# Performance work log

Measured on AMD Instinct MI355X. Metric: run time of the kernel, lower is better.

Reference implementation:

```python
import jax, jax.numpy as jnp
import numpy as np

B, S, SM, D, H, DFF = 4, 1024, 1024, 1024, 16, 4096
HD = D // H
EPS = 1e-5


def _ln(x, g, b):
    mu = jnp.mean(x, axis=-1, keepdims=True)
    var = jnp.var(x, axis=-1, keepdims=True)
    return (x - mu) * jax.lax.rsqrt(var + EPS) * g + b


def setup_inputs() -> dict:
    key = jax.random.key(0)
    ks = jax.random.split(key, 20)
    w = lambda k, shp: (0.02 * jax.random.normal(k, shp, dtype=jnp.float32))
    return {
        "tgt": jax.random.normal(ks[0], (B, S, D), dtype=jnp.float32),
        "memory": jax.random.normal(ks[1], (B, SM, D), dtype=jnp.float32),
        # self-attn (no bias)
        "Wq": w(ks[2], (D, D)), "Wk": w(ks[3], (D, D)),
        "Wv": w(ks[4], (D, D)), "Wo": w(ks[5], (D, D)),
        # cross-attn nn.MultiheadAttention params
        "mha_in_w": w(ks[6], (3 * D, D)), "mha_in_b": jnp.zeros((3 * D,), jnp.float32),
        "mha_out_w": w(ks[7], (D, D)), "mha_out_b": jnp.zeros((D,), jnp.float32),
        # FFN
        "W1": w(ks[8], (DFF, D)), "b1": jnp.zeros((DFF,), jnp.float32),
        "W2": w(ks[9], (D, DFF)), "b2": jnp.zeros((D,), jnp.float32),
        # LayerNorms
        "g1": jnp.ones((D,), jnp.float32), "be1": jnp.zeros((D,), jnp.float32),
        "g2": jnp.ones((D,), jnp.float32), "be2": jnp.zeros((D,), jnp.float32),
        "g3": jnp.ones((D,), jnp.float32), "be3": jnp.zeros((D,), jnp.float32),
    }


def _self_attn(x, Wq, Wk, Wv, Wo):
    b, s, d = x.shape
    q = (x @ Wq.T).reshape(b, s, H, HD).transpose(0, 2, 1, 3)  # [B,H,S,hd]
    k = (x @ Wk.T).reshape(b, s, H, HD).transpose(0, 2, 1, 3)
    v = (x @ Wv.T).reshape(b, s, H, HD).transpose(0, 2, 1, 3)
    scores = jnp.einsum('bhqd,bhkd->bhqk', q, k) / jnp.sqrt(jnp.float32(HD))
    mask = jnp.triu(jnp.ones((s, s), dtype=bool), k=1)  # diagonal = full_S - S + 1 = 1
    scores = jnp.where(mask, -jnp.inf, scores)
    attn = jax.nn.softmax(scores, axis=-1)
    out = jnp.einsum('bhqk,bhkd->bhqd', attn, v).transpose(0, 2, 1, 3).reshape(b, s, d)
    return out @ Wo.T, k, v


def _cross_attn(q_in, kv_in, in_w, in_b, out_w, out_b):
    Wq, Wk, Wv = jnp.split(in_w, 3, axis=0)
    bq, bk, bv = jnp.split(in_b, 3, axis=0)
    b, s, d = q_in.shape
    sm = kv_in.shape[1]
    q = (q_in @ Wq.T + bq).reshape(b, s, H, HD).transpose(0, 2, 1, 3)
    k = (kv_in @ Wk.T + bk).reshape(b, sm, H, HD).transpose(0, 2, 1, 3)
    v = (kv_in @ Wv.T + bv).reshape(b, sm, H, HD).transpose(0, 2, 1, 3)
    scores = jnp.einsum('bhqd,bhkd->bhqk', q, k) / jnp.sqrt(jnp.float32(HD))
    attn = jax.nn.softmax(scores, axis=-1)
    out = jnp.einsum('bhqk,bhkd->bhqd', attn, v).transpose(0, 2, 1, 3).reshape(b, s, d)
    return out @ out_w.T + out_b


def reference(tgt, memory, Wq, Wk, Wv, Wo, mha_in_w, mha_in_b, mha_out_w, mha_out_b,
              W1, b1, W2, b2, g1, be1, g2, be2, g3, be3):
    # dropout = 0 (eval mode)
    sa_out, sa_k, sa_v = _self_attn(_ln(tgt, g1, be1), Wq, Wk, Wv, Wo)
    x = tgt + sa_out
    ca_out = _cross_attn(_ln(x, g2, be2), memory, mha_in_w, mha_in_b, mha_out_w, mha_out_b)
    x = x + ca_out
    ff = jax.nn.relu(_ln(x, g3, be3) @ W1.T + b1) @ W2.T + b2
    x = x + ff
    return x, sa_k, sa_v
```

## Files before the change

kernel.cpp:

```cpp
#include <hip/hip_runtime.h>

typedef __bf16 bf16_t;
typedef unsigned int u32;
typedef __attribute__((ext_vector_type(8))) __bf16 bf16x8;
typedef __attribute__((ext_vector_type(4))) __bf16 bf16x4;
typedef __attribute__((ext_vector_type(4))) float f32x4;


__device__ __forceinline__ bf16x8 load8f(const float* f) {
    float4 a = *(const float4*)f;
    float4 b = *(const float4*)(f + 4);
    bf16x8 r;
    r[0] = (bf16_t)a.x; r[1] = (bf16_t)a.y; r[2] = (bf16_t)a.z; r[3] = (bf16_t)a.w;
    r[4] = (bf16_t)b.x; r[5] = (bf16_t)b.y; r[6] = (bf16_t)b.z; r[7] = (bf16_t)b.w;
    return r;
}

__device__ __forceinline__ void gll16(const void* g, const void* l) {
    __builtin_amdgcn_global_load_lds(
        (const __attribute__((address_space(1))) u32*)(unsigned long long)g,
        (__attribute__((address_space(3))) u32*)(unsigned int)(unsigned long long)l,
        16, 0, 0);
}

__global__ __launch_bounds__(256) void conv_kernel(
    const float* __restrict__ Wq, const float* __restrict__ Wk,
    const float* __restrict__ Wv, const float* __restrict__ Wo,
    const float* __restrict__ Wio, const float* __restrict__ Woo,
    const float* __restrict__ W1, const float* __restrict__ W2,
    const float* __restrict__ mem, bf16_t* __restrict__ dst)
{
    long e = ((long)blockIdx.x * 256 + threadIdx.x) * 8;
    const float* s; long o;
    if      (e <  1048576) { s = Wq;  o = e; }
    else if (e <  2097152) { s = Wk;  o = e -  1048576; }
    else if (e <  3145728) { s = Wv;  o = e -  2097152; }
    else if (e <  4194304) { s = Wo;  o = e -  3145728; }
    else if (e <  7340032) { s = Wio; o = e -  4194304; }
    else if (e <  8388608) { s = Woo; o = e -  7340032; }
    else if (e < 12582912) { s = W1;  o = e -  8388608; }
    else if (e < 16777216) { s = W2;  o = e - 12582912; }
    else                   { s = mem; o = e - 16777216; }
    *(bf16x8*)&dst[e] = load8f(s + o);
}

__global__ __launch_bounds__(256) void ln_kernel(
    const float* __restrict__ x,
    const float* __restrict__ g, const float* __restrict__ be,
    bf16_t* __restrict__ out)
{
    int row = blockIdx.x, t = threadIdx.x;
    float4 q = *(const float4*)(x + (long)row * 1024 + t * 4);
    float v[4] = {q.x, q.y, q.z, q.w};
    float s = v[0] + v[1] + v[2] + v[3];
    float s2 = v[0]*v[0] + v[1]*v[1] + v[2]*v[2] + v[3]*v[3];
    for (int off = 32; off > 0; off >>= 1) {
        s  += __shfl_down(s, off);
        s2 += __shfl_down(s2, off);
    }
    __shared__ float rs[4], rq[4];
    int w = t >> 6;
    if ((t & 63) == 0) { rs[w] = s; rq[w] = s2; }
    __syncthreads();
    s  = rs[0] + rs[1] + rs[2] + rs[3];
    s2 = rq[0] + rq[1] + rq[2] + rq[3];
    float mean = s * (1.0f / 1024.0f);
    float var  = s2 * (1.0f / 1024.0f) - mean * mean;
    float rstd = rsqrtf(var + 1e-5f);
    int c = t * 4;
    for (int i = 0; i < 4; i++)
        out[(long)row * 1024 + c + i] =
            (bf16_t)((v[i] - mean) * rstd * g[c + i] + be[c + i]);
}

template<int MI>
__global__ __launch_bounds__(512, 2) void gemm_big(
    const bf16_t* __restrict__ A, int lda,
    const bf16_t* __restrict__ Wb, long w_off, int ldw, int K,
    const float* __restrict__ bias, long b_off,
    const float* resid,
    void* o0, void* o1, void* o2, int mode, int N, int do_relu,
    void* o3, void* o4)
{
    constexpr int BM = MI << 5;
    __shared__ __align__(16) bf16_t As[2][BM * 64];
    __shared__ __align__(16) bf16_t Bs[2][256 * 64];
    int tid = threadIdx.x;
    int lin = blockIdx.y * gridDim.x + blockIdx.x;
    int mb = lin % gridDim.y, nb = lin / gridDim.y;
    int m0 = mb * BM, n0 = nb << 8;
    int w = tid >> 6, lane = tid & 63;
    int l15 = lane & 15, quad = lane >> 4;
    int wm = w >> 2, wn = w & 3;
    int srow = lane >> 3;
    int cgo  = ((lane & 7) ^ srow) << 3;

    const bf16_t* Wg = Wb + w_off;
    int nk = K >> 6;

    f32x4 acc[MI][4];
    #pragma unroll
    for (int i = 0; i < MI; i++)
        #pragma unroll
        for (int j = 0; j < 4; j++)
            acc[i][j] = (f32x4){0.f, 0.f, 0.f, 0.f};

#define STAGEB(P, KK)                                                         \
    _Pragma("unroll")                                                         \
    for (int g = 0; g < (MI >> 1); g++) {                                     \
        int rg = ((g << 3) + w) << 3;                                         \
        gll16(A  + (long)(m0 + rg + srow) * lda + (KK) + cgo, &As[P][rg << 6]); \
    }                                                                         \
    _Pragma("unroll")                                                         \
    for (int g = 0; g < 4; g++) {                                             \
        int rg = ((g << 3) + w) << 3;                                         \
        gll16(Wg + (long)(n0 + rg + srow) * ldw + (KK) + cgo, &Bs[P][rg << 6]); \
    }

    STAGEB(0, 0)
    asm volatile("s_waitcnt vmcnt(0)");
    __builtin_amdgcn_s_barrier();
    __builtin_amdgcn_sched_barrier(0);

    for (int t = 0; t < nk; t++) {
        int p = t & 1;
        bf16x8 bfr[4][2];
        #pragma unroll
        for (int q = 0; q < (MI >> 1); q++) {
            bf16x8 af[2][2];
            #pragma unroll
            for (int i2 = 0; i2 < 2; i2++)
                #pragma unroll
                for (int ks = 0; ks < 2; ks++) {
                    int row = wm * (MI << 4) + (((q << 1) + i2) << 4) + l15;
                    int sl = ((quad + (ks << 2)) ^ (l15 & 7)) << 3;
                    af[i2][ks] = *(const bf16x8*)&As[p][(row << 6) + sl];
                }
            if (q == 0) {
                #pragma unroll
                for (int j = 0; j < 4; j++)
                    #pragma unroll
                    for (int ks = 0; ks < 2; ks++) {
                        int row = (wn << 6) + (j << 4) + l15;
                        int sl = ((quad + (ks << 2)) ^ (l15 & 7)) << 3;
                        bfr[j][ks] = *(const bf16x8*)&Bs[p][(row << 6) + sl];
                    }
                if (t + 1 < nk) STAGEB(p ^ 1, (t + 1) << 6)
            }
            asm volatile("s_waitcnt lgkmcnt(0)");
            __builtin_amdgcn_sched_barrier(0);
            __builtin_amdgcn_s_setprio(1);
            #pragma unroll
            for (int i2 = 0; i2 < 2; i2++)
                #pragma unroll
                for (int j = 0; j < 4; j++)
                    #pragma unroll
                    for (int ks = 0; ks < 2; ks++)
                        acc[(q << 1) + i2][j] = __builtin_amdgcn_mfma_f32_16x16x32_bf16(
                            af[i2][ks], bfr[j][ks], acc[(q << 1) + i2][j], 0, 0, 0);
            __builtin_amdgcn_s_setprio(0);
            __builtin_amdgcn_sched_barrier(0);
        }
        if (t + 1 < nk) { asm volatile("s_waitcnt vmcnt(0)"); }
        __builtin_amdgcn_s_barrier();
        __builtin_amdgcn_sched_barrier(0);
    }
#undef STAGEB

    int rb = quad << 2;
    for (int i = 0; i < MI; i++) {
        for (int j = 0; j < 4; j++) {
            int col = n0 + (wn << 6) + (j << 4) + l15;
            float bv = bias ? bias[b_off + col] : 0.0f;
            int row0 = m0 + wm * (MI << 4) + (i << 4) + rb;
            float vv[4];
            for (int r = 0; r < 4; r++) {
                float v = acc[i][j][r] + bv;
                if (do_relu) v = fmaxf(v, 0.0f);
                vv[r] = v;
            }
            if (mode == 0) {
                for (int r = 0; r < 4; r++) {
                    int row = row0 + r;
                    long idx = (long)row * N + col;
                    float v = vv[r];
                    if (resid) v += resid[idx];
                    if (o0) ((float*)o0)[idx] = v;
                    if (o1) ((bf16_t*)o1)[idx] = (bf16_t)v;
                    if (o2) {
                        long hidx = (((long)(row >> 10) * 16 + (col >> 6)) * 1024
                                     + (row & 1023)) * 64 + (col & 63);
                        ((bf16_t*)o2)[hidx] = (bf16_t)v;
                    }
                }
            } else {
                int seg = col >> 10, c = col & 1023;
                long hb = (long)(row0 >> 10) * 16 + (c >> 6);
                long hidx0 = (hb * 1024 + (row0 & 1023)) * 64 + (c & 63);
                if (mode == 1) {
                    if (seg == 0) {
                        for (int r = 0; r < 4; r++)
                            ((bf16_t*)o0)[hidx0 + r * 64] = (bf16_t)vv[r];
                    } else if (seg == 1) {
                        for (int r = 0; r < 4; r++) {
                            ((float*)o1)[hidx0 + r * 64] = vv[r];
                            if (o3) ((bf16_t*)o3)[hidx0 + r * 64] = (bf16_t)vv[r];
                        }
                    } else {
                        for (int r = 0; r < 4; r++)
                            ((float*)o2)[hidx0 + r * 64] = vv[r];
                        if (o4) {
                            long vt0 = (hb * 64 + (c & 63)) * 1024 + (row0 & 1023);
                            bf16x4 pk;
                            for (int r = 0; r < 4; r++) pk[r] = (bf16_t)vv[r];
                            *(bf16x4*)&((bf16_t*)o4)[vt0] = pk;
                        }
                    }
                } else {
                    if (seg == 0) {
                        for (int r = 0; r < 4; r++)
                            ((bf16_t*)o0)[hidx0 + r * 64] = (bf16_t)vv[r];
                    } else {
                        long vt0 = (hb * 64 + (c & 63)) * 1024 + (row0 & 1023);
                        bf16x4 pk;
                        for (int r = 0; r < 4; r++) pk[r] = (bf16_t)vv[r];
                        *(bf16x4*)&((bf16_t*)o1)[vt0] = pk;
                    }
                }
            }
        }
    }
}

template<int NJ>
__global__ __launch_bounds__(256) void gemm_fast(
    const bf16_t* __restrict__ A, int lda, int a_head,
    const bf16_t* __restrict__ Wb, long w_off, int ldw, int K,
    const float* __restrict__ bias, long b_off,
    const float* resid,
    void* o0, void* o1, void* o2, int mode, int N, int do_relu,
    void* o3, void* o4)
{
    constexpr int BN = NJ << 5;
    __shared__ __align__(16) bf16_t As[2][128 * 64];
    __shared__ __align__(16) bf16_t Bs[2][BN * 64];
    int tid = threadIdx.x;
    int lin = blockIdx.y * gridDim.x + blockIdx.x;
    int mb = lin % gridDim.y, nb = lin / gridDim.y;
    int m0 = mb << 7, n0 = nb * BN;
    int w = tid >> 6, lane = tid & 63;
    int l15 = lane & 15, quad = lane >> 4;
    int wr = (w >> 1) << 6, wc = (w & 1) * (BN >> 1);

    int srow = lane >> 3;
    int cgo  = ((lane & 7) ^ srow) << 3;

    f32x4 acc[4][NJ];
    for (int i = 0; i < 4; i++)
        for (int j = 0; j < NJ; j++)
            acc[i][j] = (f32x4){0.f, 0.f, 0.f, 0.f};

    const bf16_t* Wg = Wb + w_off;
    int nk = K >> 6;

#define STAGE(P, KK)                                                          \
    {                                                                         \
        const bf16_t* Ab; long astr;                                          \
        if (a_head) {                                                         \
            int hh = (KK) >> 6;                                               \
            Ab = A + ((((long)(m0 >> 10)) * 16 + hh) * 1024 + (m0 & 1023)) * 64; \
            astr = 64;                                                        \
        } else {                                                              \
            Ab = A + (long)m0 * lda + (KK);                                   \
            astr = lda;                                                       \
        }                                                                     \
        const bf16_t* Bb = Wg + (long)n0 * ldw + (KK);                        \
        for (int t = 0; t < 4; t++) {                                         \
            int rb2 = (w << 5) + (t << 3);                                    \
            gll16(Ab + (long)(rb2 + srow) * astr + cgo, &As[P][rb2 << 6]);    \
        }                                                                     \
        for (int t = 0; t < NJ; t++) {                                        \
            int rb2 = w * (BN >> 2) + (t << 3);                               \
            gll16(Bb + (long)(rb2 + srow) * ldw + cgo, &Bs[P][rb2 << 6]);     \
        }                                                                     \
    }

#define COMPUTE(P)                                                            \
    for (int ks = 0; ks < 2; ks++) {                                          \
        bf16x8 af[4], bf_[NJ];                                                \
        int gA = quad + (ks << 2);                                            \
        int sl = (gA ^ (l15 & 7)) << 3;                                       \
        for (int i = 0; i < 4; i++)                                           \
            af[i]  = *(const bf16x8*)&As[P][((wr + (i << 4) + l15) << 6) + sl]; \
        for (int j = 0; j < NJ; j++)                                          \
            bf_[j] = *(const bf16x8*)&Bs[P][((wc + (j << 4) + l15) << 6) + sl]; \
        for (int i = 0; i < 4; i++)                                           \
            for (int j = 0; j < NJ; j++)                                      \
                acc[i][j] = __builtin_amdgcn_mfma_f32_16x16x32_bf16(          \
                    af[i], bf_[j], acc[i][j], 0, 0, 0);                       \
    }

    STAGE(0, 0)
    __syncthreads();
    int p = 0;
    for (int kt = 0; kt < nk; kt++) {
        if (kt + 1 < nk) STAGE(p ^ 1, (kt + 1) << 6)
        COMPUTE(p)
        __syncthreads();
        p ^= 1;
    }
#undef STAGE
#undef COMPUTE

    int rb = quad << 2;
    for (int i = 0; i < 4; i++) {
        for (int j = 0; j < NJ; j++) {
            int col = n0 + wc + (j << 4) + l15;
            float bv = bias ? bias[b_off + col] : 0.0f;
            for (int r = 0; r < 4; r++) {
                int row = m0 + wr + (i << 4) + rb + r;
                float v = acc[i][j][r] + bv;
                if (do_relu) v = fmaxf(v, 0.0f);
                if (mode == 0) {
                    long idx = (long)row * N + col;
                    if (resid) v += resid[idx];
                    if (o0) ((float*)o0)[idx] = v;
                    if (o1) ((bf16_t*)o1)[idx] = (bf16_t)v;
                    if (o2) {
                        long hidx = (((long)(row >> 10) * 16 + (col >> 6)) * 1024
                                     + (row & 1023)) * 64 + (col & 63);
                        ((bf16_t*)o2)[hidx] = (bf16_t)v;
                    }
                } else {
                    int seg = col >> 10, c = col & 1023;
                    long hidx = (((long)(row >> 10) * 16 + (c >> 6)) * 1024
                                 + (row & 1023)) * 64 + (c & 63);
                    if (mode == 1) {
                        if (seg == 0)      ((bf16_t*)o0)[hidx] = (bf16_t)v;
                        else if (seg == 1) {
                            ((float*)o1)[hidx] = v;
                            if (o3) ((bf16_t*)o3)[hidx] = (bf16_t)v;
                        } else {
                            ((float*)o2)[hidx] = v;
                            if (o4) ((bf16_t*)o4)[hidx] = (bf16_t)v;
                        }
                    } else {
                        if (seg == 0)      ((bf16_t*)o0)[hidx] = (bf16_t)v;
                        else               ((bf16_t*)o1)[hidx] = (bf16_t)v;
                    }
                }
            }
        }
    }
}

#define LDT 40

__global__ __launch_bounds__(256) void gemm_nt(
    const void* __restrict__ A, int lda, int a_head, int a_f32,
    const float* __restrict__ W, long w_off, int ldw,
    int K,
    const float* __restrict__ bias, long b_off,
    const float* __restrict__ resid,
    float*  out_f32, bf16_t* __restrict__ out_b16,
    float*  __restrict__ out_hf32, bf16_t* __restrict__ out_hb16,
    int N, int do_relu)
{
    __shared__ bf16_t As[128 * LDT];
    __shared__ bf16_t Bs[128 * LDT];
    int tid = threadIdx.x;
    int m0 = blockIdx.y << 7, n0 = blockIdx.x << 7;
    int wave = tid >> 6, lane = tid & 63;
    int wr = (wave >> 1) << 6;
    int wc = (wave & 1) << 6;
    int l15 = lane & 15, quad = lane >> 4;

    f32x4 acc[4][4];
    for (int i = 0; i < 4; i++)
        for (int j = 0; j < 4; j++)
            acc[i][j] = (f32x4){0.f, 0.f, 0.f, 0.f};

    int sr = tid >> 2;
    int sc = (tid & 3) << 3;

    for (int k0 = 0; k0 < K; k0 += 32) {
        int kk = k0 + sc;
        long ia0, ia1;
        if (a_head) {
            int hh = kk >> 6, dd = kk & 63;
            int r0g = m0 + sr, r1g = r0g + 64;
            ia0 = ((((long)(r0g >> 10) * 16 + hh) * 1024 + (r0g & 1023)) << 6) + dd;
            ia1 = ((((long)(r1g >> 10) * 16 + hh) * 1024 + (r1g & 1023)) << 6) + dd;
        } else {
            ia0 = (long)(m0 + sr) * lda + kk;
            ia1 = (long)(m0 + sr + 64) * lda + kk;
        }
        long iw0 = w_off + (long)(n0 + sr) * ldw + kk;
        long iw1 = w_off + (long)(n0 + sr + 64) * ldw + kk;
        __syncthreads();
        if (a_f32) {
            *(bf16x8*)&As[sr * LDT + sc]        = load8f((const float*)A + ia0);
            *(bf16x8*)&As[(sr + 64) * LDT + sc] = load8f((const float*)A + ia1);
        } else {
            *(bf16x8*)&As[sr * LDT + sc]        = *(const bf16x8*)((const bf16_t*)A + ia0);
            *(bf16x8*)&As[(sr + 64) * LDT + sc] = *(const bf16x8*)((const bf16_t*)A + ia1);
        }
        *(bf16x8*)&Bs[sr * LDT + sc]        = load8f(W + iw0);
        *(bf16x8*)&Bs[(sr + 64) * LDT + sc] = load8f(W + iw1);
        __syncthreads();
        bf16x8 afr[4], bfr[4];
        for (int i = 0; i < 4; i++)
            afr[i] = *(const bf16x8*)&As[(wr + i * 16 + l15) * LDT + quad * 8];
        for (int j = 0; j < 4; j++)
            bfr[j] = *(const bf16x8*)&Bs[(wc + j * 16 + l15) * LDT + quad * 8];
        for (int i = 0; i < 4; i++)
            for (int j = 0; j < 4; j++)
                acc[i][j] = __builtin_amdgcn_mfma_f32_16x16x32_bf16(
                    afr[i], bfr[j], acc[i][j], 0, 0, 0);
    }

    int rb = quad << 2;
    for (int i = 0; i < 4; i++) {
        for (int j = 0; j < 4; j++) {
            int col = n0 + wc + (j << 4) + l15;
            float bv = bias ? bias[b_off + col] : 0.0f;
            for (int r = 0; r < 4; r++) {
                int row = m0 + wr + (i << 4) + rb + r;
                float v = acc[i][j][r] + bv;
                if (do_relu) v = fmaxf(v, 0.0f);
                long idx = (long)row * N + col;
                if (resid) v += resid[idx];
                if (out_f32) out_f32[idx] = v;
                if (out_b16) out_b16[idx] = (bf16_t)v;
                if (out_hf32 || out_hb16) {
                    int bb = row >> 10, ss = row & 1023, hh = col >> 6, dd = col & 63;
                    long hidx = (((long)bb * 16 + hh) * 1024 + ss) * 64 + dd;
                    if (out_hf32) out_hf32[hidx] = v;
                    if (out_hb16) out_hb16[hidx] = (bf16_t)v;
                }
            }
        }
    }
}

__global__ __launch_bounds__(256) void attn_fast(
    const bf16_t* __restrict__ Q, const bf16_t* __restrict__ K,
    const bf16_t* __restrict__ V, bf16_t* __restrict__ AO,
    int Sk, int causal)
{
    __shared__ __align__(16) bf16_t Ks[64 * 72];
    __shared__ __align__(16) bf16_t Vt[64 * 72];
    __shared__ __align__(16) bf16_t Ps[64 * 72];

    int tid = threadIdx.x;
    int qt = blockIdx.x, bh = blockIdx.y;
    int w = tid >> 6, lane = tid & 63;
    int l15 = lane & 15, quad = lane >> 4;
    int wr = w << 4;
    int rowq = wr + (quad << 2);

    const bf16_t* Qb = Q + ((long)bh * 1024 + (qt << 6)) * 64;
    bf16x8 aq0 = *(const bf16x8*)&Qb[(wr + l15) * 64 + (quad << 3)];
    bf16x8 aq1 = *(const bf16x8*)&Qb[(wr + l15) * 64 + (quad << 3) + 32];

    float m_i[4] = {-1e30f, -1e30f, -1e30f, -1e30f};
    float l_i[4] = {0.f, 0.f, 0.f, 0.f};
    f32x4 o_acc[4];
    for (int j = 0; j < 4; j++) o_acc[j] = (f32x4){0.f, 0.f, 0.f, 0.f};

    int nt = causal ? (qt + 1) : (Sk >> 6);
    long kb = (long)bh * Sk * 64;
    long vb = (long)bh * 64 * Sk;

    int r = tid >> 2, c16 = (tid & 3) << 4;

    bf16x8 kr0, kr1, vr0, vr1;
    {
        const bf16_t* kp = K + kb + (long)r * 64 + c16;
        const bf16_t* vp = V + vb + (long)r * Sk + c16;
        kr0 = *(const bf16x8*)kp;       kr1 = *(const bf16x8*)(kp + 8);
        vr0 = *(const bf16x8*)vp;       vr1 = *(const bf16x8*)(vp + 8);
    }

    for (int kt = 0; kt < nt; kt++) {
        __syncthreads();
        *(bf16x8*)&Ks[r * 72 + c16]     = kr0;
        *(bf16x8*)&Ks[r * 72 + c16 + 8] = kr1;
        *(bf16x8*)&Vt[r * 72 + c16]     = vr0;
        *(bf16x8*)&Vt[r * 72 + c16 + 8] = vr1;
        if (kt + 1 < nt) {
            const bf16_t* kp = K + kb + (((long)(kt + 1) << 6) + r) * 64 + c16;
            const bf16_t* vp = V + vb + (long)r * Sk + ((kt + 1) << 6) + c16;
            kr0 = *(const bf16x8*)kp;   kr1 = *(const bf16x8*)(kp + 8);
            vr0 = *(const bf16x8*)vp;   vr1 = *(const bf16x8*)(vp + 8);
        }
        __syncthreads();

        f32x4 s[4];
        for (int j = 0; j < 4; j++) s[j] = (f32x4){0.f, 0.f, 0.f, 0.f};
        for (int j = 0; j < 4; j++) {
            bf16x8 bk0 = *(const bf16x8*)&Ks[((j << 4) + l15) * 72 + (quad << 3)];
            bf16x8 bk1 = *(const bf16x8*)&Ks[((j << 4) + l15) * 72 + (quad << 3) + 32];
            s[j] = __builtin_amdgcn_mfma_f32_16x16x32_bf16(aq0, bk0, s[j], 0, 0, 0);
            s[j] = __builtin_amdgcn_mfma_f32_16x16x32_bf16(aq1, bk1, s[j], 0, 0, 0);
        }

        int diag = causal && (kt == qt);
        for (int rr = 0; rr < 4; rr++) {
            float sv[4];
            for (int j = 0; j < 4; j++) {
                float x = s[j][rr] * 0.125f;
                if (diag && ((j << 4) + l15 > rowq + rr)) x = -1e30f;
                sv[j] = x;
            }
            float mx = fmaxf(fmaxf(sv[0], sv[1]), fmaxf(sv[2], sv[3]));
            for (int off = 1; off < 16; off <<= 1) mx = fmaxf(mx, __shfl_xor(mx, off));
            float mnew = fmaxf(m_i[rr], mx);
            float alpha = __expf(m_i[rr] - mnew);
            float p0 = __expf(sv[0] - mnew), p1 = __expf(sv[1] - mnew);
            float p2 = __expf(sv[2] - mnew), p3 = __expf(sv[3] - mnew);
            float rsum = p0 + p1 + p2 + p3;
            for (int off = 1; off < 16; off <<= 1) rsum += __shfl_xor(rsum, off);
            m_i[rr] = mnew;
            l_i[rr] = l_i[rr] * alpha + rsum;
            for (int j = 0; j < 4; j++) o_acc[j][rr] *= alpha;
            bf16_t* pr = &Ps[(rowq + rr) * 72 + l15];
            pr[0]  = (bf16_t)p0; pr[16] = (bf16_t)p1;
            pr[32] = (bf16_t)p2; pr[48] = (bf16_t)p3;
        }
        asm volatile("s_waitcnt lgkmcnt(0)" ::: "memory");
        __builtin_amdgcn_sched_barrier(0);

        for (int ks = 0; ks < 2; ks++) {
            int sl = (quad + (ks << 2)) << 3;
            bf16x8 ap = *(const bf16x8*)&Ps[(wr + l15) * 72 + sl];
            for (int j = 0; j < 4; j++) {
                bf16x8 bv = *(const bf16x8*)&Vt[((j << 4) + l15) * 72 + sl];
                o_acc[j] = __builtin_amdgcn_mfma_f32_16x16x32_bf16(ap, bv, o_acc[j], 0, 0, 0);
            }
        }
    }

    bf16_t* Ob = AO + ((long)bh * 1024 + (qt << 6)) * 64;
    for (int rr = 0; rr < 4; rr++) {
        float inv = 1.0f / l_i[rr];
        for (int j = 0; j < 4; j++)
            Ob[(rowq + rr) * 64 + (j << 4) + l15] = (bf16_t)(o_acc[j][rr] * inv);
    }
}

__global__ __launch_bounds__(256) void attn_kernel(
    const bf16_t* __restrict__ Q, const void* __restrict__ K,
    const void* __restrict__ V, bf16_t* __restrict__ AO,
    int Sk, int causal, int kv_f32)
{
    __shared__ __align__(16) bf16_t Qs[64 * 72];
    __shared__ __align__(16) bf16_t Ks[64 * 72];
    __shared__ __align__(16) bf16_t Vt[64 * 72];
    __shared__ __align__(16) bf16_t Ps[64 * 72];

    int tid = threadIdx.x;
    int qt = blockIdx.x, bh = blockIdx.y;
    int w = tid >> 6, lane = tid & 63;
    int l15 = lane & 15, quad = lane >> 4;
    int wr = w << 4;
    int rowq = wr + (quad << 2);

    {
        int r = tid >> 2, c16 = (tid & 3) << 4;
        const bf16_t* Qb = Q + ((long)bh * 1024 + qt * 64) * 64;
        bf16x8 a = *(const bf16x8*)&Qb[r * 64 + c16];
        bf16x8 b = *(const bf16x8*)&Qb[r * 64 + c16 + 8];
        *(bf16x8*)&Qs[r * 72 + c16] = a;
        *(bf16x8*)&Qs[r * 72 + c16 + 8] = b;
    }

    float m_i[4] = {-1e30f, -1e30f, -1e30f, -1e30f};
    float l_i[4] = {0.f, 0.f, 0.f, 0.f};
    f32x4 o_acc[4];
    for (int j = 0; j < 4; j++) o_acc[j] = (f32x4){0.f, 0.f, 0.f, 0.f};

    int nt = causal ? (qt + 1) : (Sk >> 6);
    long kvbase = (long)bh * Sk * 64;

    for (int kt = 0; kt < nt; kt++) {
        __syncthreads();
        {
            int r = tid >> 2, c16 = (tid & 3) << 4;
            long off = kvbase + (long)((kt << 6) + r) * 64 + c16;
            bf16x8 k0, k1, v0, v1;
            if (kv_f32) {
                const float* kp = (const float*)K + off;
                const float* vp = (const float*)V + off;
                k0 = load8f(kp); k1 = load8f(kp + 8);
                v0 = load8f(vp); v1 = load8f(vp + 8);
            } else {
                k0 = *(const bf16x8*)((const bf16_t*)K + off);
                k1 = *(const bf16x8*)((const bf16_t*)K + off + 8);
                v0 = *(const bf16x8*)((const bf16_t*)V + off);
                v1 = *(const bf16x8*)((const bf16_t*)V + off + 8);
            }
            *(bf16x8*)&Ks[r * 72 + c16] = k0;
            *(bf16x8*)&Ks[r * 72 + c16 + 8] = k1;
            for (int i = 0; i < 8; i++) {
                Vt[(c16 + i) * 72 + r]     = v0[i];
                Vt[(c16 + 8 + i) * 72 + r] = v1[i];
            }
        }
        __syncthreads();

        f32x4 s[4];
        for (int j = 0; j < 4; j++) s[j] = (f32x4){0.f, 0.f, 0.f, 0.f};
        for (int ks = 0; ks < 2; ks++) {
            int sl = (quad + (ks << 2)) << 3;
            bf16x8 aq = *(const bf16x8*)&Qs[(wr + l15) * 72 + sl];
            for (int j = 0; j < 4; j++) {
                bf16x8 bk = *(const bf16x8*)&Ks[((j << 4) + l15) * 72 + sl];
                s[j] = __builtin_amdgcn_mfma_f32_16x16x32_bf16(aq, bk, s[j], 0, 0, 0);
            }
        }

        int diag = causal && (kt == qt);
        for (int rr = 0; rr < 4; rr++) {
            float sv[4];
            for (int j = 0; j < 4; j++) {
                float x = s[j][rr] * 0.125f;
                if (diag && ((j << 4) + l15 > rowq + rr)) x = -1e30f;
                sv[j] = x;
            }
            float mx = fmaxf(fmaxf(sv[0], sv[1]), fmaxf(sv[2], sv[3]));
            for (int off = 1; off < 16; off <<= 1) mx = fmaxf(mx, __shfl_xor(mx, off));
            float mnew = fmaxf(m_i[rr], mx);
            float alpha = __expf(m_i[rr] - mnew);
            float p0 = __expf(sv[0] - mnew), p1 = __expf(sv[1] - mnew);
            float p2 = __expf(sv[2] - mnew), p3 = __expf(sv[3] - mnew);
            float rsum = p0 + p1 + p2 + p3;
            for (int off = 1; off < 16; off <<= 1) rsum += __shfl_xor(rsum, off);
            m_i[rr] = mnew;
            l_i[rr] = l_i[rr] * alpha + rsum;
            for (int j = 0; j < 4; j++) o_acc[j][rr] *= alpha;
            bf16_t* pr = &Ps[(rowq + rr) * 72 + l15];
            pr[0]  = (bf16_t)p0; pr[16] = (bf16_t)p1;
            pr[32] = (bf16_t)p2; pr[48] = (bf16_t)p3;
        }
        __syncthreads();

        for (int ks = 0; ks < 2; ks++) {
            int sl = (quad + (ks << 2)) << 3;
            bf16x8 ap = *(const bf16x8*)&Ps[(wr + l15) * 72 + sl];
            for (int j = 0; j < 4; j++) {
                bf16x8 bv = *(const bf16x8*)&Vt[((j << 4) + l15) * 72 + sl];
                o_acc[j] = __builtin_amdgcn_mfma_f32_16x16x32_bf16(ap, bv, o_acc[j], 0, 0, 0);
            }
        }
    }

    bf16_t* Ob = AO + ((long)bh * 1024 + qt * 64) * 64;
    for (int rr = 0; rr < 4; rr++) {
        float inv = 1.0f / l_i[rr];
        for (int j = 0; j < 4; j++)
            Ob[(rowq + rr) * 64 + (j << 4) + l15] = (bf16_t)(o_acc[j][rr] * inv);
    }
}

extern "C" void kernel_launch(void* const* d_in, const int* in_sizes, int n_in,
                              void* d_out, int out_size, void* d_ws, size_t ws_size,
                              hipStream_t stream)
{
    (void)in_sizes; (void)n_in; (void)out_size;
    const float* tgt       = (const float*)d_in[0];
    const float* mem       = (const float*)d_in[1];
    const float* Wq        = (const float*)d_in[2];
    const float* Wk        = (const float*)d_in[3];
    const float* Wv        = (const float*)d_in[4];
    const float* Wo        = (const float*)d_in[5];
    const float* mha_in_w  = (const float*)d_in[6];
    const float* mha_in_b  = (const float*)d_in[7];
    const float* mha_out_w = (const float*)d_in[8];
    const float* mha_out_b = (const float*)d_in[9];
    const float* W1        = (const float*)d_in[10];
    const float* b1        = (const float*)d_in[11];
    const float* W2        = (const float*)d_in[12];
    const float* b2        = (const float*)d_in[13];
    const float* g1        = (const float*)d_in[14];
    const float* be1       = (const float*)d_in[15];
    const float* g2        = (const float*)d_in[16];
    const float* be2       = (const float*)d_in[17];
    const float* g3        = (const float*)d_in[18];
    const float* be3       = (const float*)d_in[19];

    float* out_x = (float*)d_out;
    float* out_k = out_x + (1 << 22);
    float* out_v = out_k + (1 << 22);

    bf16_t* R0 = (bf16_t*)d_ws;
    bf16_t* R1 = R0 + (1 << 22);
    bf16_t* R2 = R1 + (1 << 22);

    dim3 blk(256);
    dim3 blk5(512);
    dim3 gA(16, 64);

    if (ws_size >= ((size_t)96 << 20)) {
        bf16_t* Hff  = R2 + (1 << 22);
        bf16_t* Wb   = (bf16_t*)((char*)d_ws + ((size_t)56 << 20));
        bf16_t* memb = Wb + 16777216;
        bf16_t* saKb = Hff;
        bf16_t* saVb = Hff + (1 << 22);
        const long WO_OFF  = 3145728;
        const long CQ_OFF  = 4194304;
        const long CKV_OFF = 5242880;
        const long CO_OFF  = 7340032;
        const long W1_OFF  = 8388608;
        const long W2_OFF  = 12582912;

        conv_kernel<<<10240, blk, 0, stream>>>(Wq, Wk, Wv, Wo, mha_in_w,
                                               mha_out_w, W1, W2, mem, Wb);

        ln_kernel<<<4096, blk, 0, stream>>>(tgt, g1, be1, R0);
        gemm_big<8><<<dim3(12, 16), blk5, 0, stream>>>(R0, 1024, Wb, 0, 1024, 1024,
                                                       nullptr, 0, nullptr,
                                                       R1, out_k, out_v, 1, 3072, 0,
                                                       saKb, saVb);
        attn_fast<<<gA, blk, 0, stream>>>(R1, saKb, saVb, R1, 1024, 1);
        gemm_fast<2><<<dim3(16, 32), blk, 0, stream>>>(R1, 0, 1, Wb, WO_OFF, 1024, 1024,
                                                       nullptr, 0, tgt,
                                                       out_x, nullptr, nullptr, 0, 1024, 0,
                                                       nullptr, nullptr);

        ln_kernel<<<4096, blk, 0, stream>>>(out_x, g2, be2, R0);
        gemm_fast<2><<<dim3(16, 32), blk, 0, stream>>>(R0, 1024, 0, Wb, CQ_OFF, 1024, 1024,
                                                       mha_in_b, 0, nullptr,
                                                       nullptr, nullptr, R1, 0, 1024, 0,
                                                       nullptr, nullptr);
        gemm_big<4><<<dim3(8, 32), blk5, 0, stream>>>(memb, 1024, Wb, CKV_OFF, 1024, 1024,
                                                      mha_in_b, 1024, nullptr,
                                                      R2, R0, nullptr, 2, 2048, 0,
                                                      nullptr, nullptr);
        attn_fast<<<gA, blk, 0, stream>>>(R1, R2, R0, R1, 1024, 0);
        gemm_fast<2><<<dim3(16, 32), blk, 0, stream>>>(R1, 0, 1, Wb, CO_OFF, 1024, 1024,
                                                       mha_out_b, 0, out_x,
                                                       out_x, nullptr, nullptr, 0, 1024, 0,
                                                       nullptr, nullptr);

        ln_kernel<<<4096, blk, 0, stream>>>(out_x, g3, be3, R0);
        gemm_big<8><<<dim3(16, 16), blk5, 0, stream>>>(R0, 1024, Wb, W1_OFF, 1024, 1024,
                                                       b1, 0, nullptr,
                                                       nullptr, Hff, nullptr, 0, 4096, 1,
                                                       nullptr, nullptr);
        gemm_fast<2><<<dim3(16, 32), blk, 0, stream>>>(Hff, 4096, 0, Wb, W2_OFF, 4096, 4096,
                                                       b2, 0, out_x,
                                                       out_x, nullptr, nullptr, 0, 1024, 0,
                                                       nullptr, nullptr);
        return;
    }

    dim3 gD(8, 32);
    dim3 gF1(32, 16);
    dim3 gF2(8, 16);

    ln_kernel<<<4096, blk, 0, stream>>>(tgt, g1, be1, R0);
    gemm_nt<<<gD, blk, 0, stream>>>(R0, 1024, 0, 0, Wq, 0, 1024, 1024,
                                    nullptr, 0, nullptr, nullptr, nullptr,
                                    nullptr, R1, 1024, 0);
    gemm_nt<<<gD, blk, 0, stream>>>(R0, 1024, 0, 0, Wk, 0, 1024, 1024,
                                    nullptr, 0, nullptr, nullptr, nullptr,
                                    out_k, nullptr, 1024, 0);
    gemm_nt<<<gD, blk, 0, stream>>>(R0, 1024, 0, 0, Wv, 0, 1024, 1024,
                                    nullptr, 0, nullptr, nullptr, nullptr,
                                    out_v, nullptr, 1024, 0);
    attn_kernel<<<gA, blk, 0, stream>>>(R1, out_k, out_v, R1, 1024, 1, 1);
    gemm_nt<<<gD, blk, 0, stream>>>(R1, 0, 1, 0, Wo, 0, 1024, 1024,
                                    nullptr, 0, tgt, out_x, nullptr,
                                    nullptr, nullptr, 1024, 0);

    ln_kernel<<<4096, blk, 0, stream>>>(out_x, g2, be2, R0);
    gemm_nt<<<gD, blk, 0, stream>>>(R0, 1024, 0, 0, mha_in_w, 0, 1024, 1024,
                                    mha_in_b, 0, nullptr, nullptr, nullptr,
                                    nullptr, R1, 1024, 0);
    gemm_nt<<<gD, blk, 0, stream>>>(mem, 1024, 0, 1, mha_in_w, (long)1 << 20, 1024, 1024,
                                    mha_in_b, 1024, nullptr, nullptr, nullptr,
                                    nullptr, R2, 1024, 0);
    gemm_nt<<<gD, blk, 0, stream>>>(mem, 1024, 0, 1, mha_in_w, (long)2 << 20, 1024, 1024,
                                    mha_in_b, 2048, nullptr, nullptr, nullptr,
                                    nullptr, R0, 1024, 0);
    attn_kernel<<<gA, blk, 0, stream>>>(R1, R2, R0, R1, 1024, 0, 0);
    gemm_nt<<<gD, blk, 0, stream>>>(R1, 0, 1, 0, mha_out_w, 0, 1024, 1024,
                                    mha_out_b, 0, out_x, out_x, nullptr,
                                    nullptr, nullptr, 1024, 0);

    ln_kernel<<<4096, blk, 0, stream>>>(out_x, g3, be3, R0);
    for (int c = 0; c < 2; c++) {
        const bf16_t* Ac = R0 + (long)c * 2048 * 1024;
        bf16_t*       Hc = R1;
        float*        Xc = out_x + (long)c * 2048 * 1024;
        gemm_nt<<<gF1, blk, 0, stream>>>(Ac, 1024, 0, 0, W1, 0, 1024, 1024,
                                         b1, 0, nullptr, nullptr, Hc,
                                         nullptr, nullptr, 4096, 1);
        gemm_nt<<<gF2, blk, 0, stream>>>(Hc, 4096, 0, 0, W2, 0, 4096, 4096,
                                         b2, 0, Xc, Xc, nullptr,
                                         nullptr, nullptr, 1024, 0);
    }
}
```

Before: 623.4 us.

## Triple-buffer GEMM LDS pipeline and use 128-row tiles for big GEMMs

Both GEMM kernels move from double to triple buffering in shared memory. Loads are issued two k-steps ahead, and partial vmcnt waits replace full drains and __syncthreads. gemm_big is specialised to 128-row tiles, so the QKV and FFN1 GEMMs launch twice as many blocks. gemm_fast also gains explicit lgkmcnt waits and setprio around its MFMA burst. The extra LDS per block (gemm_big: 144KB) may cut occupancy below the launch-bounds target, and the smaller M tile lowers reuse of each B tile.

New measurement: 600.9 us. 3.6% less time.

```diff
diff --git a/kernel.cpp b/kernel.cpp
--- a/kernel.cpp
+++ b/kernel.cpp
@@ -73,8 +73,7 @@
             (bf16_t)((v[i] - mean) * rstd * g[c + i] + be[c + i]);
 }
 
-template<int MI>
-__global__ __launch_bounds__(512, 2) void gemm_big(
+__global__ __launch_bounds__(512, 2) void gemm_big128(
     const bf16_t* __restrict__ A, int lda,
     const bf16_t* __restrict__ Wb, long w_off, int ldw, int K,
     const float* __restrict__ bias, long b_off,
@@ -82,13 +81,12 @@
     void* o0, void* o1, void* o2, int mode, int N, int do_relu,
     void* o3, void* o4)
 {
-    constexpr int BM = MI << 5;
-    __shared__ __align__(16) bf16_t As[2][BM * 64];
-    __shared__ __align__(16) bf16_t Bs[2][256 * 64];
+    __shared__ __align__(16) bf16_t As[3][128 * 64];
+    __shared__ __align__(16) bf16_t Bs[3][256 * 64];
     int tid = threadIdx.x;
     int lin = blockIdx.y * gridDim.x + blockIdx.x;
     int mb = lin % gridDim.y, nb = lin / gridDim.y;
-    int m0 = mb * BM, n0 = nb << 8;
+    int m0 = mb << 7, n0 = nb << 8;
     int w = tid >> 6, lane = tid & 63;
     int l15 = lane & 15, quad = lane >> 4;
     int wm = w >> 2, wn = w & 3;
@@ -98,16 +96,16 @@
     const bf16_t* Wg = Wb + w_off;
     int nk = K >> 6;
 
-    f32x4 acc[MI][4];
+    f32x4 acc[4][4];
     #pragma unroll
-    for (int i = 0; i < MI; i++)
+    for (int i = 0; i < 4; i++)
         #pragma unroll
         for (int j = 0; j < 4; j++)
             acc[i][j] = (f32x4){0.f, 0.f, 0.f, 0.f};
 
 #define STAGEB(P, KK)                                                         \
     _Pragma("unroll")                                                         \
-    for (int g = 0; g < (MI >> 1); g++) {                                     \
+    for (int g = 0; g < 2; g++) {                                             \
         int rg = ((g << 3) + w) << 3;                                         \
         gll16(A  + (long)(m0 + rg + srow) * lda + (KK) + cgo, &As[P][rg << 6]); \
     }                                                                         \
@@ -118,21 +116,24 @@
     }
 
     STAGEB(0, 0)
-    asm volatile("s_waitcnt vmcnt(0)");
+    if (nk > 1) STAGEB(1, 64)
+    if (nk > 1) { asm volatile("s_waitcnt vmcnt(6)"); }
+    else        { asm volatile("s_waitcnt vmcnt(0)"); }
+    __builtin_amdgcn_sched_barrier(0);
     __builtin_amdgcn_s_barrier();
     __builtin_amdgcn_sched_barrier(0);
 
+    int p = 0;
     for (int t = 0; t < nk; t++) {
-        int p = t & 1;
         bf16x8 bfr[4][2];
         #pragma unroll
-        for (int q = 0; q < (MI >> 1); q++) {
+        for (int q = 0; q < 2; q++) {
             bf16x8 af[2][2];
             #pragma unroll
             for (int i2 = 0; i2 < 2; i2++)
                 #pragma unroll
                 for (int ks = 0; ks < 2; ks++) {
-                    int row = wm * (MI << 4) + (((q << 1) + i2) << 4) + l15;
+                    int row = (wm << 6) + (((q << 1) + i2) << 4) + l15;
                     int sl = ((quad + (ks << 2)) ^ (l15 & 7)) << 3;
                     af[i2][ks] = *(const bf16x8*)&As[p][(row << 6) + sl];
                 }
@@ -145,7 +146,10 @@
                         int sl = ((quad + (ks << 2)) ^ (l15 & 7)) << 3;
                         bfr[j][ks] = *(const bf16x8*)&Bs[p][(row << 6) + sl];
                     }
-                if (t + 1 < nk) STAGEB(p ^ 1, (t + 1) << 6)
+                if (t + 2 < nk) {
+                    int s2 = (p + 2 >= 3) ? p - 1 : p + 2;
+                    STAGEB(s2, (t + 2) << 6)
+                }
             }
             asm volatile("s_waitcnt lgkmcnt(0)");
             __builtin_amdgcn_sched_barrier(0);
@@ -161,18 +165,21 @@
             __builtin_amdgcn_s_setprio(0);
             __builtin_amdgcn_sched_barrier(0);
         }
-        if (t + 1 < nk) { asm volatile("s_waitcnt vmcnt(0)"); }
+        if (t + 2 < nk)      { asm volatile("s_waitcnt vmcnt(6)"); }
+        else if (t + 1 < nk) { asm volatile("s_waitcnt vmcnt(0)"); }
+        __builtin_amdgcn_sched_barrier(0);
         __builtin_amdgcn_s_barrier();
         __builtin_amdgcn_sched_barrier(0);
+        p = (p == 2) ? 0 : p + 1;
     }
 #undef STAGEB
 
     int rb = quad << 2;
-    for (int i = 0; i < MI; i++) {
+    for (int i = 0; i < 4; i++) {
         for (int j = 0; j < 4; j++) {
             int col = n0 + (wn << 6) + (j << 4) + l15;
             float bv = bias ? bias[b_off + col] : 0.0f;
-            int row0 = m0 + wm * (MI << 4) + (i << 4) + rb;
+            int row0 = m0 + (wm << 6) + (i << 4) + rb;
             float vv[4];
             for (int r = 0; r < 4; r++) {
                 float v = acc[i][j][r] + bv;
@@ -242,8 +249,8 @@
     void* o3, void* o4)
 {
     constexpr int BN = NJ << 5;
-    __shared__ __align__(16) bf16_t As[2][128 * 64];
-    __shared__ __align__(16) bf16_t Bs[2][BN * 64];
+    __shared__ __align__(16) bf16_t As[3][128 * 64];
+    __shared__ __align__(16) bf16_t Bs[3][BN * 64];
     int tid = threadIdx.x;
     int lin = blockIdx.y * gridDim.x + blockIdx.x;
     int mb = lin % gridDim.y, nb = lin / gridDim.y;
@@ -294,20 +301,38 @@
             af[i]  = *(const bf16x8*)&As[P][((wr + (i << 4) + l15) << 6) + sl]; \
         for (int j = 0; j < NJ; j++)                                          \
             bf_[j] = *(const bf16x8*)&Bs[P][((wc + (j << 4) + l15) << 6) + sl]; \
+        asm volatile("s_waitcnt lgkmcnt(0)");                                 \
+        __builtin_amdgcn_sched_barrier(0);                                    \
+        __builtin_amdgcn_s_setprio(1);                                        \
         for (int i = 0; i < 4; i++)                                           \
             for (int j = 0; j < NJ; j++)                                      \
                 acc[i][j] = __builtin_amdgcn_mfma_f32_16x16x32_bf16(          \
                     af[i], bf_[j], acc[i][j], 0, 0, 0);                       \
+        __builtin_amdgcn_s_setprio(0);                                        \
+        __builtin_amdgcn_sched_barrier(0);                                    \
     }
 
     STAGE(0, 0)
-    __syncthreads();
+    if (nk > 1) STAGE(1, 64)
+    if (nk > 1) { asm volatile("s_waitcnt vmcnt(6)"); }
+    else        { asm volatile("s_waitcnt vmcnt(0)"); }
+    __builtin_amdgcn_sched_barrier(0);
+    __builtin_amdgcn_s_barrier();
+    __builtin_amdgcn_sched_barrier(0);
+
     int p = 0;
     for (int kt = 0; kt < nk; kt++) {
-        if (kt + 1 < nk) STAGE(p ^ 1, (kt + 1) << 6)
+        if (kt + 2 < nk) {
+            int s2 = (p + 2 >= 3) ? p - 1 : p + 2;
+            STAGE(s2, (kt + 2) << 6)
+        }
         COMPUTE(p)
-        __syncthreads();
-        p ^= 1;
+        if (kt + 2 < nk)      { asm volatile("s_waitcnt vmcnt(6)"); }
+        else if (kt + 1 < nk) { asm volatile("s_waitcnt vmcnt(0)"); }
+        __builtin_amdgcn_sched_barrier(0);
+        __builtin_amdgcn_s_barrier();
+        __builtin_amdgcn_sched_barrier(0);
+        p = (p == 2) ? 0 : p + 1;
     }
 #undef STAGE
 #undef COMPUTE
@@ -718,7 +743,7 @@
                                                mha_out_w, W1, W2, mem, Wb);
 
         ln_kernel<<<4096, blk, 0, stream>>>(tgt, g1, be1, R0);
-        gemm_big<8><<<dim3(12, 16), blk5, 0, stream>>>(R0, 1024, Wb, 0, 1024, 1024,
+        gemm_big128<<<dim3(12, 32), blk5, 0, stream>>>(R0, 1024, Wb, 0, 1024, 1024,
                                                        nullptr, 0, nullptr,
                                                        R1, out_k, out_v, 1, 3072, 0,
                                                        saKb, saVb);
@@ -733,7 +758,7 @@
                                                        mha_in_b, 0, nullptr,
                                                        nullptr, nullptr, R1, 0, 1024, 0,
                                                        nullptr, nullptr);
-        gemm_big<4><<<dim3(8, 32), blk5, 0, stream>>>(memb, 1024, Wb, CKV_OFF, 1024, 1024,
+        gemm_big128<<<dim3(8, 32), blk5, 0, stream>>>(memb, 1024, Wb, CKV_OFF, 1024, 1024,
                                                       mha_in_b, 1024, nullptr,
                                                       R2, R0, nullptr, 2, 2048, 0,
                                                       nullptr, nullptr);
@@ -744,7 +769,7 @@
                                                        nullptr, nullptr);
 
         ln_kernel<<<4096, blk, 0, stream>>>(out_x, g3, be3, R0);
-        gemm_big<8><<<dim3(16, 16), blk5, 0, stream>>>(R0, 1024, Wb, W1_OFF, 1024, 1024,
+        gemm_big128<<<dim3(16, 32), blk5, 0, stream>>>(R0, 1024, Wb, W1_OFF, 1024, 1024,
                                                        b1, 0, nullptr,
                                                        nullptr, Hff, nullptr, 0, 4096, 1,
                                                        nullptr, nullptr);
```
